# Performance work log

Measured on AMD Instinct MI355X. Metric: run time of the kernel, lower is better.

Reference implementation:

```python
import jax, jax.numpy as jnp
import numpy as np

SOS_TOKEN = 2
T = 1024      # sequence / max_length
H = 256       # embedding_dim == GRU hidden size
V = 50000     # vocab_size


def gru_cell(e, h, w_ih, w_hh, b_ih, b_hh):
    # PyTorch nn.GRU cell math. e, h: [H]; w_ih, w_hh: [3H, H]; b_*: [3H]
    gi = w_ih @ e + b_ih
    gh = w_hh @ h + b_hh
    i_r, i_z, i_n = jnp.split(gi, 3)
    h_r, h_z, h_n = jnp.split(gh, 3)
    r = jax.nn.sigmoid(i_r + h_r)
    z = jax.nn.sigmoid(i_z + h_z)
    n = jnp.tanh(i_n + r * h_n)
    return (1.0 - z) * n + z * h


def setup_inputs() -> dict:
    key = jax.random.key(0)
    ks = jax.random.split(key, 14)
    s = 1.0 / np.sqrt(H)
    def u(k, shape):
        return jax.random.uniform(k, shape, jnp.float32, -s, s)
    return {
        "x": jax.random.randint(ks[0], (T,), 0, V),
        "enc_emb": jax.random.normal(ks[1], (V, H), jnp.float32),
        "enc_w_ih": u(ks[2], (3 * H, H)),
        "enc_w_hh": u(ks[3], (3 * H, H)),
        "enc_b_ih": u(ks[4], (3 * H,)),
        "enc_b_hh": u(ks[5], (3 * H,)),
        "dec_emb": jax.random.normal(ks[6], (V, H), jnp.float32),
        "dec_w_ih": u(ks[7], (3 * H, H)),
        "dec_w_hh": u(ks[8], (3 * H, H)),
        "dec_b_ih": u(ks[9], (3 * H,)),
        "dec_b_hh": u(ks[10], (3 * H,)),
        "w_out": u(ks[11], (V, H)),
        "b_out": u(ks[12], (V,)),
    }


def reference(x, enc_emb, enc_w_ih, enc_w_hh, enc_b_ih, enc_b_hh,
              dec_emb, dec_w_ih, dec_w_hh, dec_b_ih, dec_b_hh, w_out, b_out):
    # ---- Encoder: embed whole sequence, scan GRU to final hidden ----
    emb_seq = enc_emb[x]                      # [T, H] (no relu in encoder)

    def enc_step(h, e):
        return gru_cell(e, h, enc_w_ih, enc_w_hh, enc_b_ih, enc_b_hh), None

    h_enc, _ = jax.lax.scan(enc_step, jnp.zeros((H,), emb_seq.dtype), emb_seq)

    # ---- Decoder: greedy argmax feedback, per-step log-softmax ----
    def dec_step(carry, _):
        h, tok = carry
        e = jax.nn.relu(dec_emb[tok])         # embed + relu
        h = gru_cell(e, h, dec_w_ih, dec_w_hh, dec_b_ih, dec_b_hh)
        logits = w_out @ h + b_out            # [V]
        logp = jax.nn.log_softmax(logits)
        tok = jnp.argmax(logp)                # topk(1) greedy feedback
        return (h, tok), logp

    init = (h_enc, jnp.asarray(SOS_TOKEN, x.dtype))
    _, decoder_outputs = jax.lax.scan(dec_step, init, None, length=T)
    return decoder_outputs                    # [T, V] log-probs
```

## Files before the change

### kernel.cpp

```cpp
#include <hip/hip_runtime.h>
#include <stdint.h>

#define TSEQ 1024
#define H 256
#define H3 768
#define NV 50000
#define NBLK 256
#define NTHR 512
#define RPB 196
#define SOS_TOK 2
#define SPIN_LIM (1 << 20)
#define NEB_L 64
#define NEW 4
#define EEL 64
#define EROWS 192

#define WS_SALT   0
#define WS_DISP   64
#define WS_ROSTER 128
#define WS_VERD   832
#define WS_HENC   1024
#define WS_PMX    8192
#define WS_REC    16384
#define WS_EHL2   32768
#define WS_GIENC  65536
#define WS_TABLE  (65536 + TSEQ * H3 * 4)
#define TABLE_BYTES ((size_t)NV * H3 * 4)

using u64 = unsigned long long;

__device__ __forceinline__ void awr(u64* p, u64 v) {
  __hip_atomic_store(p, v, __ATOMIC_RELAXED, __HIP_MEMORY_SCOPE_AGENT);
}
__device__ __forceinline__ u64 ard(u64* p) {
  return __hip_atomic_load(p, __ATOMIC_RELAXED, __HIP_MEMORY_SCOPE_AGENT);
}
__device__ __forceinline__ unsigned ard32(unsigned* p) {
  return __hip_atomic_load(p, __ATOMIC_RELAXED, __HIP_MEMORY_SCOPE_AGENT);
}
__device__ __forceinline__ u64 pkf(unsigned tg, float f) {
  return ((u64)tg << 32) | (u64)__float_as_uint(f);
}
__device__ __forceinline__ u64 pku(unsigned tg, unsigned v) {
  return ((u64)tg << 32) | (u64)v;
}
__device__ __forceinline__ float upf(u64 w) { return __uint_as_float((unsigned)w); }
__device__ __forceinline__ unsigned tagof(u64 w) { return (unsigned)(w >> 32); }

__device__ __forceinline__ void wgst(u64* p, u64 v) {
  __hip_atomic_store(p, v, __ATOMIC_RELAXED, __HIP_MEMORY_SCOPE_WORKGROUP);
}
__device__ __forceinline__ u64 wgld(u64* p) {
  u64 v;
  asm volatile("global_atomic_add_x2 %0, %1, %2, off sc0\n\ts_waitcnt vmcnt(0)"
               : "=v"(v) : "v"(p), "v"(0ull) : "memory");
  return v;
}

__device__ __forceinline__ void agpr_w(float& dst, float v) {
  asm volatile("v_accvgpr_write_b32 %0, %1" : "=a"(dst) : "v"(v));
}
__device__ __forceinline__ float agpr_r(float src) {
  float v;
  asm volatile("v_accvgpr_read_b32 %0, %1" : "=v"(v) : "a"(src));
  return v;
}

extern "C" __global__ void k_init(char* ws) {
  if (threadIdx.x == 0) {
    unsigned* s = (unsigned*)(ws + WS_SALT);
    *s = *s + 1u;
    *(unsigned*)(ws + WS_DISP) = 0u;
    for (int i = 0; i < 8; ++i) *(unsigned*)(ws + WS_ROSTER + i * 64) = 0u;
  }
}

extern "C" __global__ void k_enc_gi(const int* __restrict__ x, const float* __restrict__ emb,
                                    const float* __restrict__ wih, const float* __restrict__ bih,
                                    float* __restrict__ gi) {
  int tid = threadIdx.x;
  int t0 = blockIdx.x * 16;
  __shared__ float4 se4[16][H / 4];
  float* se = (float*)se4;
  for (int idx = tid; idx < 16 * H; idx += 256) {
    int j = idx >> 8, k = idx & 255;
    se[j * H + k] = emb[(size_t)x[t0 + j] * H + k];
  }
  __syncthreads();
  for (int q = 0; q < 3; q++) {
    int r = q * H + tid;
    const float4* w4 = (const float4*)(wih + (size_t)r * H);
    float bb = bih[r];
    float a[16];
#pragma unroll
    for (int j = 0; j < 16; j++) a[j] = bb;
    for (int k = 0; k < H / 4; k++) {
      float4 wv = w4[k];
#pragma unroll
      for (int j = 0; j < 16; j++) {
        float4 ev = se4[j][k];
        a[j] += wv.x * ev.x + wv.y * ev.y + wv.z * ev.z + wv.w * ev.w;
      }
    }
#pragma unroll
    for (int j = 0; j < 16; j++) gi[(size_t)(t0 + j) * H3 + r] = a[j];
  }
}

extern "C" __global__ void __launch_bounds__(NTHR, 1)
k_enc(const float* __restrict__ enc_whh, const float* __restrict__ enc_bhh,
      const float* __restrict__ dec_emb, const float* __restrict__ dec_wih,
      const float* __restrict__ dec_bih, char* __restrict__ ws, int use_table) {
  const int b = blockIdx.x, tid = threadIdx.x;
  u64* henc = (u64*)(ws + WS_HENC);
  u64* ehl2 = (u64*)(ws + WS_EHL2);
  u64* verd = (u64*)(ws + WS_VERD);
  const float* gi_enc = (const float*)(ws + WS_GIENC);
  float* table = (float*)(ws + WS_TABLE);

  __shared__ float se[16 * H];
  __shared__ float sh_h[H];
  __shared__ float sh_ghE[EROWS];
  __shared__ int sh_xcd, sh_rank, sh_chosen, sh_u, sh_abort;
  if (tid == 0) sh_abort = 0;

  const unsigned salt = *(volatile unsigned*)(ws + WS_SALT);
  const unsigned tb32 = salt * 65536u;

  if (tid == 0) {
    unsigned x;
    asm volatile("s_getreg_b32 %0, hwreg(HW_REG_XCC_ID)" : "=s"(x));
    int myxcd = (int)(x & 7u);
    unsigned* rost = (unsigned*)(ws + WS_ROSTER);
    int rank = (int)__hip_atomic_fetch_add(rost + myxcd * 16, 1u,
                                           __ATOMIC_RELAXED, __HIP_MEMORY_SCOPE_AGENT);
    long n_ = 0;
    unsigned tot = 0;
    do {
      tot = 0;
      for (int i = 0; i < 8; ++i) tot += ard32(rost + i * 16);
      if (++n_ > 2000000L) break;
      __builtin_amdgcn_s_sleep(1);
    } while (tot < (unsigned)NEB_L);
    int chosen = -1;
    for (int i = 0; i < 8; ++i) {
      unsigned c = ard32(rost + i * 16);
      if (chosen < 0 && c >= (unsigned)NEW) chosen = i;
    }
    sh_xcd = myxcd; sh_rank = rank; sh_chosen = chosen;
  }
  __syncthreads();
  bool isw;
  int role;
  if (sh_chosen >= 0) { isw = (sh_xcd == sh_chosen) && (sh_rank < NEW); role = sh_rank; }
  else { isw = (b < NEW); role = b; }

  if (!isw) {
    if (!use_table) return;
    unsigned* disp = (unsigned*)(ws + WS_DISP);
    for (;;) {
      if (tid == 0)
        sh_u = (int)__hip_atomic_fetch_add(disp, 1u, __ATOMIC_RELAXED,
                                           __HIP_MEMORY_SCOPE_AGENT);
      __syncthreads();
      int u = sh_u;
      if (u >= NV / 16) return;
      int v0 = u * 16;
      for (int idx = tid; idx < 16 * H; idx += NTHR) {
        int j = idx >> 8, k2 = idx & 255;
        se[j * H + k2] = fmaxf(dec_emb[(size_t)(v0 + j) * H + k2], 0.f);
      }
      __syncthreads();
      for (int r = tid; r < H3; r += NTHR) {
        const float4* w4 = (const float4*)(dec_wih + (size_t)r * H);
        float bb = dec_bih[r];
        float a[16];
#pragma unroll
        for (int j = 0; j < 16; j++) a[j] = bb;
        for (int k = 0; k < H / 4; k++) {
          float4 wv = w4[k];
#pragma unroll
          for (int j = 0; j < 16; j++) {
            const float4 ev = ((const float4*)se)[j * (H / 4) + k];
            a[j] += wv.x * ev.x + wv.y * ev.y + wv.z * ev.z + wv.w * ev.w;
          }
        }
#pragma unroll
        for (int j = 0; j < 16; j++)
          table[(size_t)(v0 + j) * H3 + r] = a[j];
      }
      __syncthreads();
    }
  }

  const int el = role * EEL + (tid & 63);
  const int elw = role * EEL + tid;

  int okl = 1;
  for (int k = 0; k < 8 && okl; ++k) {
    unsigned wtg = tb32 + 50001u + (unsigned)k;
    if (tid < EEL) wgst(ehl2 + (size_t)(k & 1) * 256 + elw, pku(wtg, 0u));
    int lim = (k == 0) ? 6000 : 2000;
    int myok = 1;
    if (tid < H) {
      u64* pp_ = ehl2 + (size_t)(k & 1) * 256 + tid;
      u64 w = 0; int n_ = 0;
      do { w = wgld(pp_); } while (tagof(w) != wtg && ++n_ < lim);
      myok = (tagof(w) == wtg);
    }
    okl = __syncthreads_and(myok);
  }
  const unsigned tagV = tb32 + 60001u;
  if (tid == 0) awr(verd + role, pku(tagV, okl ? 0u : 1u));
  int fb = 0;
  if (tid < NEW) {
    u64 w = 0; int n_ = 0;
    do { w = ard(verd + tid); } while (tagof(w) != tagV && ++n_ < SPIN_LIM);
    fb = (tagof(w) != tagV) ? 1 : (int)(w & 1u);
  }
  const bool l2m = __syncthreads_and(fb == 0);
  u64* EX = l2m ? ehl2 : henc;

  const int p2 = tid >> 1, hf = tid & 1;
  const bool ract = (p2 < EROWS);
  const int q = p2 >> 6, ri = p2 & 63;
  const size_t grow = ract ? (size_t)(q * H + role * EEL + ri) : 0;
  float wa[128];
  {
    const float4* wp = (const float4*)(enc_whh + grow * H + hf * 128);
#pragma unroll
    for (int k = 0; k < 32; ++k) {
      float4 v = ract ? wp[k] : make_float4(0.f, 0.f, 0.f, 0.f);
      agpr_w(wa[4 * k + 0], v.x);
      agpr_w(wa[4 * k + 1], v.y);
      agpr_w(wa[4 * k + 2], v.z);
      agpr_w(wa[4 * k + 3], v.w);
    }
  }
  float be0 = 0.f, be1 = 0.f, be2 = 0.f;
  if (tid < EEL) { be0 = enc_bhh[el]; be1 = enc_bhh[H + el]; be2 = enc_bhh[2 * H + el]; }
  __syncthreads();

  float hb = 0.f;
  if (tid < EEL) {
    float g0 = gi_enc[el], g1 = gi_enc[H + el], g2 = gi_enc[2 * H + el];
    float r = 1.f / (1.f + expf(-(g0 + be0)));
    float z = 1.f / (1.f + expf(-(g1 + be1)));
    float n = tanhf(g2 + r * be2);
    hb = (1.f - z) * n;
    u64 w = pkf(tb32 + 1u, hb);
    if (l2m) wgst(EX + 256 + elw, w); else awr(EX + 256 + elw, w);
  }
  int ec = 1;
  for (int t = 1; t < TSEQ; ++t) {
    float g0 = 0.f, g1 = 0.f, g2 = 0.f;
    if (tid < EEL) {
      g0 = gi_enc[(size_t)t * H3 + el];
      g1 = gi_enc[(size_t)t * H3 + H + el];
      g2 = gi_enc[(size_t)t * H3 + 2 * H + el];
    }
    if (tid < H) {
      u64* pp_ = EX + (size_t)(ec & 1) * 256 + tid;
      u64 w = 0; int n_ = 0;
      if (l2m) { do { w = wgld(pp_); } while (tagof(w) != tb32 + (unsigned)ec && ++n_ < SPIN_LIM); }
      else     { do { w = ard(pp_); }  while (tagof(w) != tb32 + (unsigned)ec && ++n_ < SPIN_LIM); }
      if (tagof(w) != tb32 + (unsigned)ec) sh_abort = 1;
      sh_h[tid] = upf(w);
    }
    __syncthreads();
    if (sh_abort) return;
    float pcc = 0.f;
    if (ract) {
      const float4* h4 = ((const float4*)sh_h) + hf * 32;
#pragma unroll
      for (int k = 0; k < 32; ++k) {
        float4 hv = h4[k];
        pcc += agpr_r(wa[4 * k + 0]) * hv.x + agpr_r(wa[4 * k + 1]) * hv.y +
               agpr_r(wa[4 * k + 2]) * hv.z + agpr_r(wa[4 * k + 3]) * hv.w;
      }
    }
    pcc += __shfl_xor(pcc, 1);
    if (ract && hf == 0) sh_ghE[p2] = pcc;
    __syncthreads();
    ++ec;
    if (tid < EEL) {
      float r = 1.f / (1.f + expf(-(g0 + (sh_ghE[tid] + be0))));
      float z = 1.f / (1.f + expf(-(g1 + (sh_ghE[EEL + tid] + be1))));
      float n = tanhf(g2 + r * (sh_ghE[2 * EEL + tid] + be2));
      hb = (1.f - z) * n + z * hb;
      u64 w = pkf(tb32 + (unsigned)ec, hb);
      u64* d = EX + (size_t)(ec & 1) * 256 + elw;
      if (l2m) wgst(d, w); else awr(d, w);
    }
  }
  if (l2m && tid < EEL) awr(henc + elw, pkf(tb32 + (unsigned)TSEQ, hb));
}

extern "C" __global__ void __launch_bounds__(NTHR, 1)
k_dec(const float* __restrict__ dec_emb, const float* __restrict__ dec_wih,
      const float* __restrict__ dec_whh, const float* __restrict__ dec_bih,
      const float* __restrict__ dec_bhh, const float* __restrict__ w_out,
      const float* __restrict__ b_out, float* __restrict__ out,
      char* __restrict__ ws, int use_table) {
  const int b = blockIdx.x, tid = threadIdx.x;
  u64* henc = (u64*)(ws + WS_HENC);
  u64* pmx = (u64*)(ws + WS_PMX);
  u64* rec = (u64*)(ws + WS_REC);
  const float* table = (const float*)(ws + WS_TABLE);

  __shared__ float sh_h[H];
  __shared__ float sh_wd[3][H];
  __shared__ float sh_wi[3][H];
  __shared__ float sh_gi[H3];
  __shared__ float gh_lds[H3];
  __shared__ float sh_lg[2][RPB];
  __shared__ float sh_bout[RPB];
  __shared__ float sh_gh3[3];
  __shared__ float sh_rv[8];
  __shared__ float sh_mv[8];
  __shared__ int sh_mi[8];
  __shared__ float sh_sv[8];
  __shared__ float sh_mv2[8];
  __shared__ int sh_mi2[8];
  __shared__ float sh_sv2[8];
  __shared__ float sh_e[H];
  __shared__ int sh_abort;

  if (tid == 0) sh_abort = 0;

  for (int k = tid; k < 3 * H; k += NTHR) {
    int q = k >> 8, c = k & 255;
    sh_wd[q][c] = dec_whh[((size_t)(3 * b + q)) * H + c];
    if (!use_table) sh_wi[q][c] = dec_wih[((size_t)(3 * b + q)) * H + c];
  }
  const float bd0 = dec_bhh[3 * b], bd1 = dec_bhh[3 * b + 1], bd2 = dec_bhh[3 * b + 2];
  float bi0 = 0.f, bi1 = 0.f, bi2 = 0.f;
  if (!use_table) { bi0 = dec_bih[3 * b]; bi1 = dec_bih[3 * b + 1]; bi2 = dec_bih[3 * b + 2]; }
  const int rowbase = b * RPB;
  const int nrows = min(RPB, max(0, NV - rowbase));
  const int p = tid >> 1, hf = tid & 1;
  const bool wact = (p < nrows);
  float wa[128];
  {
    const float4* wp = (const float4*)(w_out + (size_t)(rowbase + (wact ? p : 0)) * H + hf * 128);
#pragma unroll
    for (int i = 0; i < 32; ++i) {
      float4 v = wact ? wp[i] : make_float4(0.f, 0.f, 0.f, 0.f);
      agpr_w(wa[4 * i + 0], v.x);
      agpr_w(wa[4 * i + 1], v.y);
      agpr_w(wa[4 * i + 2], v.z);
      agpr_w(wa[4 * i + 3], v.w);
    }
  }
  if (tid < RPB) sh_bout[tid] = (tid < nrows) ? b_out[rowbase + tid] : 0.f;
  const unsigned salt = *(volatile unsigned*)(ws + WS_SALT);
  const unsigned tb32 = salt * 65536u;
  const unsigned tb24 = salt * 4096u;
  __syncthreads();

  auto wave_maxidx = [&](float& mv, int& mi) {
#pragma unroll
    for (int off = 32; off >= 1; off >>= 1) {
      float ov = __shfl_xor(mv, off);
      int oi = __shfl_xor(mi, off);
      if (ov > mv || (ov == mv && oi < mi)) { mv = ov; mi = oi; }
    }
  };
  auto row3 = [&](const float(&wr)[3][H], float bb0, float bb1, float bb2, const float* vin) {
    int q = tid >> 7, i = tid & 127;
    float pp = 0.f;
    if (q < 3) pp = wr[q][2 * i] * vin[2 * i] + wr[q][2 * i + 1] * vin[2 * i + 1];
#pragma unroll
    for (int off = 32; off >= 1; off >>= 1) pp += __shfl_xor(pp, off);
    if (q < 3 && (tid & 63) == 0) sh_rv[tid >> 6] = pp;
    __syncthreads();
    if (tid == 0) {
      sh_gh3[0] = sh_rv[0] + sh_rv[1] + bb0;
      sh_gh3[1] = sh_rv[2] + sh_rv[3] + bb1;
      sh_gh3[2] = sh_rv[4] + sh_rv[5] + bb2;
    }
    __syncthreads();
  };
  auto gru_step = [&]() {
    if (tid < H) {
      float gir = sh_gi[tid], giz = sh_gi[H + tid], gin = sh_gi[2 * H + tid];
      float ghr = gh_lds[tid], ghz = gh_lds[H + tid], ghn = gh_lds[2 * H + tid];
      float r = 1.f / (1.f + expf(-(gir + ghr)));
      float z = 1.f / (1.f + expf(-(giz + ghz)));
      float n = tanhf(gin + r * ghn);
      sh_h[tid] = (1.f - z) * n + z * sh_h[tid];
    }
    __syncthreads();
  };
  auto spin_rec3 = [&](unsigned tg, float* dst) {
    if (tid < NBLK) {
      u64* pp_ = rec + (size_t)(tg & 1) * 1024 + (size_t)tid * 4;
      u64 w0 = 0, w1 = 0, w2 = 0; int n = 0; bool ok;
      do {
        w0 = ard(pp_ + 0); w1 = ard(pp_ + 1); w2 = ard(pp_ + 2);
        ok = (tagof(w0) == tg) & (tagof(w1) == tg) & (tagof(w2) == tg);
      } while (!ok && ++n < SPIN_LIM);
      if (!ok) sh_abort = 1;
      dst[3 * tid] = upf(w0); dst[3 * tid + 1] = upf(w1); dst[3 * tid + 2] = upf(w2);
    }
    __syncthreads();
  };

  if (tid < NBLK) {
    u64* pp_ = henc + tid;
    u64 w = 0; int n_ = 0;
    do { w = ard(pp_); } while (tagof(w) != tb32 + (unsigned)TSEQ && ++n_ < SPIN_LIM);
    if (tagof(w) != tb32 + (unsigned)TSEQ) sh_abort = 1;
    sh_h[tid] = upf(w);
  }
  __syncthreads();
  if (sh_abort) return;

  int e = TSEQ;
  row3(sh_wd, bd0, bd1, bd2, sh_h);
  ++e;
  {
    unsigned tg = tb32 + (unsigned)e;
    if (tid == 0) {
      u64* d = rec + (size_t)(tg & 1) * 1024 + (size_t)b * 4;
      awr(d + 0, pkf(tg, sh_gh3[0]));
      awr(d + 1, pkf(tg, sh_gh3[1]));
      awr(d + 2, pkf(tg, sh_gh3[2]));
    }
    spin_rec3(tg, gh_lds);
    if (sh_abort) return;
  }

  int tok = SOS_TOK;
  float2 gp = make_float2(0.f, 0.f);
  if (use_table) {
    if (tid < 384) gp = *(const float2*)(table + (size_t)SOS_TOK * H3 + 2 * tid);
  } else {
    for (int j = tid; j < H; j += NTHR) sh_e[j] = fmaxf(dec_emb[(size_t)SOS_TOK * H + j], 0.f);
    __syncthreads();
    row3(sh_wi, bi0, bi1, bi2, sh_e);
    ++e;
    unsigned tg = tb32 + (unsigned)e;
    if (tid == 0) {
      u64* d = rec + (size_t)(tg & 1) * 1024 + (size_t)b * 4;
      awr(d + 0, pkf(tg, sh_gh3[0]));
      awr(d + 1, pkf(tg, sh_gh3[1]));
      awr(d + 2, pkf(tg, sh_gh3[2]));
    }
    spin_rec3(tg, sh_gi);
    if (sh_abort) return;
  }

  float sv_p = 0.f, bm_p = -INFINITY, gm_p = 0.f;
  for (int t = 0; t < TSEQ; ++t) {
    const int cur = t & 1;
    if (use_table) {
      if (tid < 384) { sh_gi[2 * tid] = gp.x; sh_gi[2 * tid + 1] = gp.y; }
    }
    __syncthreads();
    gru_step();
    float acc = 0.f;
    if (wact) {
      const float4* h4 = ((const float4*)sh_h) + hf * 32;
#pragma unroll
      for (int i = 0; i < 32; ++i) {
        float4 hv = h4[i];
        acc += agpr_r(wa[4 * i + 0]) * hv.x + agpr_r(wa[4 * i + 1]) * hv.y +
               agpr_r(wa[4 * i + 2]) * hv.z + agpr_r(wa[4 * i + 3]) * hv.w;
      }
    }
    acc += __shfl_xor(acc, 1);
    if (wact && hf == 0) sh_lg[cur][p] = acc + sh_bout[p];
    __syncthreads();
    ++e;
    const unsigned tg32 = tb32 + (unsigned)e;
    const unsigned tg24 = (tb24 + (unsigned)e) & 0xFFFFFFu;
    float mv = (tid < nrows) ? sh_lg[cur][tid] : -INFINITY;
    int mi = (tid < nrows) ? (rowbase + tid) : 0x7fffffff;
    wave_maxidx(mv, mi);
    if ((tid & 63) == 0) { sh_mv[tid >> 6] = mv; sh_mi[tid >> 6] = mi; }
    __syncthreads();
    float bmax = sh_mv[0]; int bidx = sh_mi[0];
#pragma unroll
    for (int k = 1; k < 8; ++k)
      if (sh_mv[k] > bmax || (sh_mv[k] == bmax && sh_mi[k] < bidx)) { bmax = sh_mv[k]; bidx = sh_mi[k]; }
    if (tid == 0) {
      u64 g = ((u64)tg24 << 40) | ((u64)__float_as_uint(bmax) << 8) |
              (u64)((unsigned)(bidx - rowbase) & 0xFFu);
      awr(pmx + (size_t)(e & 1) * 256 + b, g);
    }
    row3(sh_wd, bd0, bd1, bd2, sh_h);
    if (tid == 0) {
      u64* d = rec + (size_t)(e & 1) * 1024 + (size_t)b * 4;
      awr(d + 0, pkf(tg32, sh_gh3[0]));
      awr(d + 1, pkf(tg32, sh_gh3[1]));
      awr(d + 2, pkf(tg32, sh_gh3[2]));
    }
    float ec = (tid < nrows) ? __expf(sh_lg[cur][tid] - bmax) : 0.f;
#pragma unroll
    for (int off = 32; off >= 1; off >>= 1) ec += __shfl_xor(ec, off);
    if ((tid & 63) == 0) sh_sv[tid >> 6] = ec;
    __syncthreads();
    float bsum = 0.f;
#pragma unroll
    for (int k = 0; k < 8; ++k) bsum += sh_sv[k];
    if (tid == 0)
      awr(rec + (size_t)(e & 1) * 1024 + (size_t)b * 4 + 3, pkf(tg32, bsum));
    if (t > 0) {
      float c = (tid < NBLK) ? sv_p * __expf(bm_p - gm_p) : 0.f;
#pragma unroll
      for (int off = 32; off >= 1; off >>= 1) c += __shfl_xor(c, off);
      if ((tid & 63) == 0) sh_sv2[tid >> 6] = c;
      __syncthreads();
      float S = 0.f;
#pragma unroll
      for (int k = 0; k < 8; ++k) S += sh_sv2[k];
      float lse = gm_p + logf(S);
      if (tid < nrows)
        out[(size_t)(t - 1) * NV + rowbase + tid] = sh_lg[cur ^ 1][tid] - lse;
    }
    float bm_e = -INFINITY; int ie = 0x7fffffff;
    {
      u64 w = 0;
      if (tid < NBLK) {
        u64* pp_ = pmx + (size_t)(e & 1) * 256 + tid;
        int n = 0;
        do { w = ard(pp_); } while ((unsigned)(w >> 40) != tg24 && ++n < SPIN_LIM);
        if ((unsigned)(w >> 40) != tg24) sh_abort = 1;
        bm_e = __uint_as_float((unsigned)((w >> 8) & 0xFFFFFFFFu));
        ie = tid * RPB + (int)(w & 0xFFu);
      }
      __syncthreads();
      if (sh_abort) return;
    }
    float mv2 = bm_e; int mi2 = ie;
    wave_maxidx(mv2, mi2);
    if ((tid & 63) == 0) { sh_mv2[tid >> 6] = mv2; sh_mi2[tid >> 6] = mi2; }
    __syncthreads();
    float gmax = sh_mv2[0]; int gidx = sh_mi2[0];
#pragma unroll
    for (int k = 1; k < 8; ++k)
      if (sh_mv2[k] > gmax || (sh_mv2[k] == gmax && sh_mi2[k] < gidx)) { gmax = sh_mv2[k]; gidx = sh_mi2[k]; }
    tok = gidx;
    if (use_table && t + 1 < TSEQ) {
      if (tid < 384) gp = *(const float2*)(table + (size_t)tok * H3 + 2 * tid);
    }
    float sv = 0.f;
    if (tid < NBLK) {
      u64* pp_ = rec + (size_t)(e & 1) * 1024 + (size_t)tid * 4;
      u64 w0 = 0, w1 = 0, w2 = 0, w3 = 0; int n = 0; bool ok;
      do {
        w0 = ard(pp_ + 0); w1 = ard(pp_ + 1); w2 = ard(pp_ + 2); w3 = ard(pp_ + 3);
        ok = (tagof(w0) == tg32) & (tagof(w1) == tg32) & (tagof(w2) == tg32) &
             (tagof(w3) == tg32);
      } while (!ok && ++n < SPIN_LIM);
      if (!ok) sh_abort = 1;
      gh_lds[3 * tid] = upf(w0); gh_lds[3 * tid + 1] = upf(w1); gh_lds[3 * tid + 2] = upf(w2);
      sv = upf(w3);
    }
    __syncthreads();
    if (sh_abort) return;
    sv_p = sv; bm_p = bm_e; gm_p = gmax;
    if (!use_table && t + 1 < TSEQ) {
      for (int j = tid; j < H; j += NTHR) sh_e[j] = fmaxf(dec_emb[(size_t)tok * H + j], 0.f);
      __syncthreads();
      row3(sh_wi, bi0, bi1, bi2, sh_e);
      ++e;
      unsigned tgg = tb32 + (unsigned)e;
      if (tid == 0) {
        u64* d = rec + (size_t)(tgg & 1) * 1024 + (size_t)b * 4;
        awr(d + 0, pkf(tgg, sh_gh3[0]));
        awr(d + 1, pkf(tgg, sh_gh3[1]));
        awr(d + 2, pkf(tgg, sh_gh3[2]));
      }
      spin_rec3(tgg, sh_gi);
      if (sh_abort) return;
    }
  }
  {
    float c = (tid < NBLK) ? sv_p * __expf(bm_p - gm_p) : 0.f;
#pragma unroll
    for (int off = 32; off >= 1; off >>= 1) c += __shfl_xor(c, off);
    if ((tid & 63) == 0) sh_sv2[tid >> 6] = c;
    __syncthreads();
    float S = 0.f;
#pragma unroll
    for (int k = 0; k < 8; ++k) S += sh_sv2[k];
    float lse = gm_p + logf(S);
    if (tid < nrows)
      out[(size_t)(TSEQ - 1) * NV + rowbase + tid] = sh_lg[(TSEQ - 1) & 1][tid] - lse;
  }
}

extern "C" void kernel_launch(void* const* d_in, const int* in_sizes, int n_in,
                              void* d_out, int out_size, void* d_ws, size_t ws_size,
                              hipStream_t stream) {
  (void)in_sizes; (void)n_in; (void)out_size;
  const int* x = (const int*)d_in[0];
  const float* enc_emb = (const float*)d_in[1];
  const float* enc_wih = (const float*)d_in[2];
  const float* enc_whh = (const float*)d_in[3];
  const float* enc_bih = (const float*)d_in[4];
  const float* enc_bhh = (const float*)d_in[5];
  const float* dec_emb = (const float*)d_in[6];
  const float* dec_wih = (const float*)d_in[7];
  const float* dec_whh = (const float*)d_in[8];
  const float* dec_bih = (const float*)d_in[9];
  const float* dec_bhh = (const float*)d_in[10];
  const float* w_out = (const float*)d_in[11];
  const float* b_out = (const float*)d_in[12];
  float* out = (float*)d_out;
  char* ws = (char*)d_ws;

  int use_table = (ws_size >= (size_t)WS_TABLE + TABLE_BYTES) ? 1 : 0;

  k_init<<<1, 64, 0, stream>>>(ws);
  k_enc_gi<<<TSEQ / 16, 256, 0, stream>>>(x, enc_emb, enc_wih, enc_bih, (float*)(ws + WS_GIENC));
  k_enc<<<NEB_L, NTHR, 0, stream>>>(enc_whh, enc_bhh, dec_emb, dec_wih, dec_bih, ws, use_table);
  k_dec<<<NBLK, NTHR, 0, stream>>>(dec_emb, dec_wih, dec_whh, dec_bih, dec_bhh,
                                   w_out, b_out, out, ws, use_table);
}
```

Baseline: 8.644 ms.

## Overlap argmax and record polling across wave halves, cutting per-step grid barriers

Restructures the decoder step so the argmax-partial poll and the gh/sum record poll run concurrently in separate thread halves, instead of as two sequential spin phases each followed by a block sync. Each block also publishes its local max in a separate slot so the softmax correction can use it. The recurrent gh dot products and the exp-sum now run in dedicated waves without an extra __syncthreads, and the previous step's log-softmax write is moved after the merged poll. The aim is to shorten the serial critical path of each of the 1024 greedy steps. The cost is one extra atomic publish and poll per block per step, plus tighter coupling of roles across waves.

After: 12.97 ms. 1.5x slower.

```diff
diff --git a/kernel.cpp b/kernel.cpp
--- a/kernel.cpp
+++ b/kernel.cpp
@@ -21,6 +21,7 @@
 #define WS_VERD   832
 #define WS_HENC   1024
 #define WS_PMX    8192
+#define WS_BMX    12288
 #define WS_REC    16384
 #define WS_EHL2   32768
 #define WS_GIENC  65536
@@ -305,6 +306,7 @@
   const int b = blockIdx.x, tid = threadIdx.x;
   u64* henc = (u64*)(ws + WS_HENC);
   u64* pmx = (u64*)(ws + WS_PMX);
+  u64* bmx = (u64*)(ws + WS_BMX);
   u64* rec = (u64*)(ws + WS_REC);
   const float* table = (const float*)(ws + WS_TABLE);
 
@@ -451,6 +453,7 @@
     if (sh_abort) return;
   }
 
+  const int wv = tid >> 6, ln = tid & 63;
   float sv_p = 0.f, bm_p = -INFINITY, gm_p = 0.f;
   for (int t = 0; t < TSEQ; ++t) {
     const int cur = t & 1;
@@ -478,7 +481,7 @@
     float mv = (tid < nrows) ? sh_lg[cur][tid] : -INFINITY;
     int mi = (tid < nrows) ? (rowbase + tid) : 0x7fffffff;
     wave_maxidx(mv, mi);
-    if ((tid & 63) == 0) { sh_mv[tid >> 6] = mv; sh_mi[tid >> 6] = mi; }
+    if (ln == 0) { sh_mv[wv] = mv; sh_mi[wv] = mi; }
     __syncthreads();
     float bmax = sh_mv[0]; int bidx = sh_mi[0];
 #pragma unroll
@@ -488,79 +491,80 @@
       u64 g = ((u64)tg24 << 40) | ((u64)__float_as_uint(bmax) << 8) |
               (u64)((unsigned)(bidx - rowbase) & 0xFFu);
       awr(pmx + (size_t)(e & 1) * 256 + b, g);
-    }
-    row3(sh_wd, bd0, bd1, bd2, sh_h);
-    if (tid == 0) {
-      u64* d = rec + (size_t)(e & 1) * 1024 + (size_t)b * 4;
-      awr(d + 0, pkf(tg32, sh_gh3[0]));
-      awr(d + 1, pkf(tg32, sh_gh3[1]));
-      awr(d + 2, pkf(tg32, sh_gh3[2]));
-    }
-    float ec = (tid < nrows) ? __expf(sh_lg[cur][tid] - bmax) : 0.f;
-#pragma unroll
-    for (int off = 32; off >= 1; off >>= 1) ec += __shfl_xor(ec, off);
-    if ((tid & 63) == 0) sh_sv[tid >> 6] = ec;
-    __syncthreads();
-    float bsum = 0.f;
-#pragma unroll
-    for (int k = 0; k < 8; ++k) bsum += sh_sv[k];
-    if (tid == 0)
-      awr(rec + (size_t)(e & 1) * 1024 + (size_t)b * 4 + 3, pkf(tg32, bsum));
-    if (t > 0) {
-      float c = (tid < NBLK) ? sv_p * __expf(bm_p - gm_p) : 0.f;
-#pragma unroll
-      for (int off = 32; off >= 1; off >>= 1) c += __shfl_xor(c, off);
-      if ((tid & 63) == 0) sh_sv2[tid >> 6] = c;
-      __syncthreads();
-      float S = 0.f;
-#pragma unroll
-      for (int k = 0; k < 8; ++k) S += sh_sv2[k];
-      float lse = gm_p + logf(S);
-      if (tid < nrows)
-        out[(size_t)(t - 1) * NV + rowbase + tid] = sh_lg[cur ^ 1][tid] - lse;
+      awr(bmx + (size_t)(e & 1) * 256 + b, pkf(tg32, bmax));
     }
     float bm_e = -INFINITY; int ie = 0x7fffffff;
-    {
-      u64 w = 0;
-      if (tid < NBLK) {
-        u64* pp_ = pmx + (size_t)(e & 1) * 256 + tid;
-        int n = 0;
-        do { w = ard(pp_); } while ((unsigned)(w >> 40) != tg24 && ++n < SPIN_LIM);
-        if ((unsigned)(w >> 40) != tg24) sh_abort = 1;
-        bm_e = __uint_as_float((unsigned)((w >> 8) & 0xFFFFFFFFu));
-        ie = tid * RPB + (int)(w & 0xFFu);
-      }
-      __syncthreads();
-      if (sh_abort) return;
-    }
-    float mv2 = bm_e; int mi2 = ie;
-    wave_maxidx(mv2, mi2);
-    if ((tid & 63) == 0) { sh_mv2[tid >> 6] = mv2; sh_mi2[tid >> 6] = mi2; }
-    __syncthreads();
+    float sv_n = 0.f, bm_n = -INFINITY;
+    if (wv < 3) {
+      float pp = 0.f;
+      const float* wr = sh_wd[wv];
+      int c0 = 4 * ln;
+#pragma unroll
+      for (int j = 0; j < 4; ++j) pp += wr[c0 + j] * sh_h[c0 + j];
+#pragma unroll
+      for (int off = 32; off >= 1; off >>= 1) pp += __shfl_xor(pp, off);
+      if (ln == 0) {
+        float bb = (wv == 0) ? bd0 : ((wv == 1) ? bd1 : bd2);
+        awr(rec + (size_t)(e & 1) * 1024 + (size_t)b * 4 + wv, pkf(tg32, pp + bb));
+      }
+    } else if (wv == 3) {
+      float s = 0.f;
+#pragma unroll
+      for (int j = 0; j < 4; ++j) {
+        int r2 = ln + 64 * j;
+        if (r2 < nrows) s += __expf(sh_lg[cur][r2] - bmax);
+      }
+#pragma unroll
+      for (int off = 32; off >= 1; off >>= 1) s += __shfl_xor(s, off);
+      if (ln == 0)
+        awr(rec + (size_t)(e & 1) * 1024 + (size_t)b * 4 + 3, pkf(tg32, s));
+    }
+    if (tid < NBLK) {
+      u64* pp_ = pmx + (size_t)(e & 1) * 256 + tid;
+      u64 w = 0; int n = 0;
+      do { w = ard(pp_); } while ((unsigned)(w >> 40) != tg24 && ++n < SPIN_LIM);
+      if ((unsigned)(w >> 40) != tg24) sh_abort = 1;
+      bm_e = __uint_as_float((unsigned)((w >> 8) & 0xFFFFFFFFu));
+      ie = tid * RPB + (int)(w & 0xFFu);
+      wave_maxidx(bm_e, ie);
+      if (ln == 0) { sh_mv2[wv] = bm_e; sh_mi2[wv] = ie; }
+    } else {
+      int r2 = tid - NBLK;
+      u64* pp_ = rec + (size_t)(e & 1) * 1024 + (size_t)r2 * 4;
+      u64* pb_ = bmx + (size_t)(e & 1) * 256 + r2;
+      u64 w0 = 0, w1 = 0, w2 = 0, w3 = 0, w4 = 0; int n = 0; bool ok;
+      do {
+        w0 = ard(pp_ + 0); w1 = ard(pp_ + 1); w2 = ard(pp_ + 2); w3 = ard(pp_ + 3);
+        w4 = ard(pb_);
+        ok = (tagof(w0) == tg32) & (tagof(w1) == tg32) & (tagof(w2) == tg32) &
+             (tagof(w3) == tg32) & (tagof(w4) == tg32);
+      } while (!ok && ++n < SPIN_LIM);
+      if (!ok) sh_abort = 1;
+      gh_lds[3 * r2] = upf(w0); gh_lds[3 * r2 + 1] = upf(w1); gh_lds[3 * r2 + 2] = upf(w2);
+      sv_n = upf(w3); bm_n = upf(w4);
+    }
+    __syncthreads();
+    if (sh_abort) return;
     float gmax = sh_mv2[0]; int gidx = sh_mi2[0];
 #pragma unroll
-    for (int k = 1; k < 8; ++k)
+    for (int k = 1; k < 4; ++k)
       if (sh_mv2[k] > gmax || (sh_mv2[k] == gmax && sh_mi2[k] < gidx)) { gmax = sh_mv2[k]; gidx = sh_mi2[k]; }
     tok = gidx;
     if (use_table && t + 1 < TSEQ) {
       if (tid < 384) gp = *(const float2*)(table + (size_t)tok * H3 + 2 * tid);
     }
-    float sv = 0.f;
-    if (tid < NBLK) {
-      u64* pp_ = rec + (size_t)(e & 1) * 1024 + (size_t)tid * 4;
-      u64 w0 = 0, w1 = 0, w2 = 0, w3 = 0; int n = 0; bool ok;
-      do {
-        w0 = ard(pp_ + 0); w1 = ard(pp_ + 1); w2 = ard(pp_ + 2); w3 = ard(pp_ + 3);
-        ok = (tagof(w0) == tg32) & (tagof(w1) == tg32) & (tagof(w2) == tg32) &
-             (tagof(w3) == tg32);
-      } while (!ok && ++n < SPIN_LIM);
-      if (!ok) sh_abort = 1;
-      gh_lds[3 * tid] = upf(w0); gh_lds[3 * tid + 1] = upf(w1); gh_lds[3 * tid + 2] = upf(w2);
-      sv = upf(w3);
-    }
-    __syncthreads();
-    if (sh_abort) return;
-    sv_p = sv; bm_p = bm_e; gm_p = gmax;
+    if (t > 0) {
+      float c = (tid >= NBLK) ? sv_p * __expf(bm_p - gm_p) : 0.f;
+#pragma unroll
+      for (int off = 32; off >= 1; off >>= 1) c += __shfl_xor(c, off);
+      if (tid >= NBLK && ln == 0) sh_sv2[wv - 4] = c;
+      __syncthreads();
+      float S = ((sh_sv2[0] + sh_sv2[1]) + sh_sv2[2]) + sh_sv2[3];
+      float lse = gm_p + logf(S);
+      if (tid < nrows)
+        out[(size_t)(t - 1) * NV + rowbase + tid] = sh_lg[cur ^ 1][tid] - lse;
+    }
+    sv_p = sv_n; bm_p = bm_n; gm_p = gmax;
     if (!use_table && t + 1 < TSEQ) {
       for (int j = tid; j < H; j += NTHR) sh_e[j] = fmaxf(dec_emb[(size_t)tok * H + j], 0.f);
       __syncthreads();
@@ -578,14 +582,12 @@
     }
   }
   {
-    float c = (tid < NBLK) ? sv_p * __expf(bm_p - gm_p) : 0.f;
+    float c = (tid >= NBLK) ? sv_p * __expf(bm_p - gm_p) : 0.f;
 #pragma unroll
     for (int off = 32; off >= 1; off >>= 1) c += __shfl_xor(c, off);
-    if ((tid & 63) == 0) sh_sv2[tid >> 6] = c;
-    __syncthreads();
-    float S = 0.f;
-#pragma unroll
-    for (int k = 0; k < 8; ++k) S += sh_sv2[k];
+    if (tid >= NBLK && ln == 0) sh_sv2[wv - 4] = c;
+    __syncthreads();
+    float S = ((sh_sv2[0] + sh_sv2[1]) + sh_sv2[2]) + sh_sv2[3];
     float lse = gm_p + logf(S);
     if (tid < nrows)
       out[(size_t)(TSEQ - 1) * NV + rowbase + tid] = sh_lg[(TSEQ - 1) & 1][tid] - lse;
```
